# Performance work log

Measured on AMD Instinct MI355X. Metric: run time of the kernel, lower is better.

## Reference

```python
import jax, jax.numpy as jnp
import numpy as np

B, A, N = 8, 512, 64           # structures, atoms, neighbors
D, F, G = 128, 128, 25         # atom basis, filters, gaussians
L = 3                          # interaction blocks
GA = 512                       # angular feature dim = 2*n_zetas*2*n_angular*n_zetas
MAXZ = 100
CUTOFF, START = 5.0, 1.2
LN2 = 0.6931471805599453


def ssp(x):
    # shifted softplus: ln(1+exp(x)) - ln(2)
    return jax.nn.softplus(x) - LN2


def setup_inputs() -> dict:
    key = jax.random.key(0)
    ks = jax.random.split(key, 16)
    atomic_numbers = jax.random.randint(ks[0], (B, A), 0, MAXZ, dtype=jnp.int32)
    positions = jax.random.normal(ks[1], (B, A, 3), dtype=jnp.float32) * 3.0
    neighbors = jax.random.randint(ks[2], (B, A, N), 0, A, dtype=jnp.int32)
    neighbor_mask = jax.random.randint(ks[3], (B, A, N), 0, 2, dtype=jnp.int32)
    G_i = jax.random.normal(ks[4], (B, A, GA), dtype=jnp.float32)
    s = 0.05
    embedding = jax.random.normal(ks[5], (MAXZ, D), dtype=jnp.float32) * 0.1
    embedding = embedding.at[0].set(0.0)  # padding_idx=0
    inp = {
        'atomic_numbers': atomic_numbers,
        'positions': positions,
        'neighbors': neighbors,
        'neighbor_mask': neighbor_mask,
        'G_i': G_i,
        'embedding': embedding,
        'filt_w1': jax.random.normal(ks[6], (L, G, F), dtype=jnp.float32) * s,
        'filt_b1': jnp.zeros((L, F), jnp.float32),
        'filt_w2': jax.random.normal(ks[7], (L, F, F), dtype=jnp.float32) * s,
        'filt_b2': jnp.zeros((L, F), jnp.float32),
        'in2f_w': jax.random.normal(ks[8], (L, D, F), dtype=jnp.float32) * s,
        'f2out_w': jax.random.normal(ks[9], (L, F, D), dtype=jnp.float32) * s,
        'f2out_b': jnp.zeros((L, D), jnp.float32),
        'dense_w': jax.random.normal(ks[10], (L, D, D), dtype=jnp.float32) * s,
        'dense_b': jnp.zeros((L, D), jnp.float32),
        'ang_w': jax.random.normal(ks[11], (L, GA, D), dtype=jnp.float32) * s,
    }
    return inp


def reference(atomic_numbers, positions, neighbors, neighbor_mask, G_i,
              embedding, filt_w1, filt_b1, filt_w2, filt_b2,
              in2f_w, f2out_w, f2out_b, dense_w, dense_b, ang_w):
    gather = jax.vmap(lambda feat, idx: feat[idx])  # per-structure neighbor gather

    x = embedding[atomic_numbers]                    # [B,A,D]

    # AtomDistances: gather neighbor positions and take pairwise norms
    pos_j = gather(positions, neighbors)             # [B,A,N,3]
    dvec = pos_j - positions[:, :, None, :]
    r_ij = jnp.sqrt(jnp.sum(dvec * dvec, axis=-1) + 1e-12)  # [B,A,N]

    # GaussianSmearing(start, cutoff, n_gaussians)
    offsets = jnp.linspace(START, CUTOFF, G).astype(x.dtype)
    width = offsets[1] - offsets[0]
    f_ij = jnp.exp((-0.5 / (width * width)) * (r_ij[..., None] - offsets) ** 2)  # [B,A,N,G]

    C = (r_ij <= CUTOFF).astype(x.dtype)             # HardCutoff [B,A,N]
    mask = neighbor_mask.astype(x.dtype)             # [B,A,N]

    for l in range(in2f_w.shape[0]):
        # filter-generating network on expanded distances, modulated by cutoff
        W = ssp(f_ij @ filt_w1[l] + filt_b1[l]) @ filt_w2[l] + filt_b2[l]  # [B,A,N,F]
        W = W * C[..., None]
        # CFConv: project, gather neighbors, filter-weight, masked neighbor sum
        y = x @ in2f_w[l]                            # [B,A,F]
        y_j = gather(y, neighbors)                   # [B,A,N,F]
        agg = jnp.sum(y_j * W * mask[..., None], axis=2)  # [B,A,F]
        v_rad = agg @ f2out_w[l] + f2out_b[l]        # f2out (activation=None)
        v_rad = v_rad @ dense_w[l] + dense_b[l]      # self.dense
        v_ang = G_i @ ang_w[l]                       # dense_angular (no bias)
        x = x + ssp(v_rad + v_ang)                   # residual interaction update
    return x
```

## Files before the change

### kernel.cpp

```cpp
#include <hip/hip_runtime.h>
#include <math.h>

#define NB 8
#define NA 512
#define NN 64
#define ND 128
#define NF 128
#define NG 25
#define NGA 512
#define TABN 1024

typedef __attribute__((ext_vector_type(8))) short bf16x8;
typedef __attribute__((ext_vector_type(4))) float f32x4;

__device__ __forceinline__ float sspf(float v) {
  return fmaxf(v, 0.0f) + __logf(1.0f + __expf(-fabsf(v))) - 0.6931471805599453f;
}

__device__ __forceinline__ short f2bf(float x) {
  union { float f; unsigned u; } v; v.f = x;
  unsigned r = v.u + 0x7fffu + ((v.u >> 16) & 1u);
  return (short)(r >> 16);
}

#if defined(__has_builtin)
#if __has_builtin(__builtin_amdgcn_cvt_pk_bf16_f32)
#define HAS_PKBF 1
#endif
#endif

__device__ __forceinline__ unsigned pk2bf(float a, float b) {
#ifdef HAS_PKBF
  typedef __attribute__((ext_vector_type(2))) __bf16 v2bf;
  union { v2bf v; unsigned u; } c;
  c.v = __builtin_amdgcn_cvt_pk_bf16_f32(a, b);
  return c.u;
#else
  union { float f; unsigned u; } x, y; x.f = a; y.f = b;
  const unsigned ra = (x.u + 0x7fffu + ((x.u >> 16) & 1u)) >> 16;
  const unsigned rb = (y.u + 0x7fffu + ((y.u >> 16) & 1u)) & 0xffff0000u;
  return ra | rb;
#endif
}

__device__ __forceinline__ float bf2f(unsigned short us) {
  union { unsigned u; float f; } v; v.u = ((unsigned)us) << 16; return v.f;
}

__device__ __forceinline__ bf16x8 pack8(float4 a, float4 b) {
  bf16x8 r;
  unsigned* p = (unsigned*)&r;
  p[0] = pk2bf(a.x, a.y); p[1] = pk2bf(a.z, a.w);
  p[2] = pk2bf(b.x, b.y); p[3] = pk2bf(b.z, b.w);
  return r;
}

__device__ __forceinline__ bf16x8 fragT(const float* __restrict__ M, int ldn,
                                        int n, int k0q) {
  float e[8];
#pragma unroll
  for (int i = 0; i < 8; ++i) e[i] = M[(size_t)(k0q + i) * ldn + n];
  bf16x8 r; unsigned* p = (unsigned*)&r;
  p[0] = pk2bf(e[0], e[1]); p[1] = pk2bf(e[2], e[3]);
  p[2] = pk2bf(e[4], e[5]); p[3] = pk2bf(e[6], e[7]);
  return r;
}

__device__ __forceinline__ bf16x8 fragT25(const float* __restrict__ M,
                                          int n, int k0q) {
  float e[8];
#pragma unroll
  for (int i = 0; i < 8; ++i)
    e[i] = (k0q + i < NG) ? M[(size_t)(k0q + i) * NF + n] : 0.0f;
  bf16x8 r; unsigned* p = (unsigned*)&r;
  p[0] = pk2bf(e[0], e[1]); p[1] = pk2bf(e[2], e[3]);
  p[2] = pk2bf(e[4], e[5]); p[3] = pk2bf(e[6], e[7]);
  return r;
}

#define B_TT 48
#define B_AT (B_TT + 192)
#define B_PF (B_AT + 24)
#define B_TAB (B_PF + 192)
#define P1_TOT (B_TAB + 1024)

__global__ __launch_bounds__(256) void k_prep1(
    const float* __restrict__ fw1, const float* __restrict__ fb1,
    const float* __restrict__ fw2, const float* __restrict__ fb2,
    const float* __restrict__ in2f, const float* __restrict__ aw,
    const float* __restrict__ f2o, const float* __restrict__ f2ob,
    const float* __restrict__ dw, const float* __restrict__ db,
    const float* __restrict__ pos, const int* __restrict__ nbr,
    const int* __restrict__ nmask,
    short* __restrict__ in2fT, short* __restrict__ awT,
    short* __restrict__ W12T, float* __restrict__ b12,
    float* __restrict__ Ttab, int4* __restrict__ ent,
    int* __restrict__ nvArr) {
  __shared__ alignas(16) short sTile[32][33];
  __shared__ alignas(16) short sH[16 * 136];
  __shared__ alignas(16) int4 sCmp[4][NN];
  const int bx = blockIdx.x;
  const int t = threadIdx.x;
  const int lane = t & 63, wave = t >> 6;
  const int lanelo = lane & 15, quad = lane >> 4;
  const int wbase = wave << 5;

  if (bx < B_AT) {
    const float* src; short* dst; int tk0, tn0, stride;
    if (bx < B_TT) {
      const int l = bx >> 4, tile = bx & 15;
      src = in2f + (size_t)l * 16384;
      dst = in2fT + (size_t)l * 16384;
      tk0 = (tile >> 2) << 5; tn0 = (tile & 3) << 5; stride = 128;
    } else {
      const int ab = bx - B_TT;
      const int l = ab >> 6, tile = ab & 63;
      src = aw + (size_t)l * 65536;
      dst = awT + (size_t)l * 65536;
      tk0 = (tile >> 2) << 5; tn0 = (tile & 3) << 5; stride = 512;
    }
    const int tr = t >> 3, tc4 = (t & 7) << 2;
    const float4 v = *(const float4*)(src + (size_t)(tk0 + tr) * 128 + tn0 + tc4);
    sTile[tr][tc4] = f2bf(v.x); sTile[tr][tc4 + 1] = f2bf(v.y);
    sTile[tr][tc4 + 2] = f2bf(v.z); sTile[tr][tc4 + 3] = f2bf(v.w);
    __syncthreads();
    short o[4];
#pragma unroll
    for (int j = 0; j < 4; ++j) o[j] = sTile[tc4 + j][tr];
    uint2 pk;
    pk.x = ((unsigned)(unsigned short)o[0]) | (((unsigned)(unsigned short)o[1]) << 16);
    pk.y = ((unsigned)(unsigned short)o[2]) | (((unsigned)(unsigned short)o[3]) << 16);
    *(uint2*)(dst + (size_t)(tn0 + tr) * stride + tk0 + tc4) = pk;
    return;
  }
  if (bx < B_PF) {
    const int fb = bx - B_AT;
    const int l = fb >> 3, xi = fb & 7;
    const int i = (xi << 4) + lanelo;
    const float* f2o_l = f2o + (size_t)l * 16384;
    const float* dw_l = dw + (size_t)l * 16384;
    short* W12T_l = W12T + (size_t)l * 16384;
    f32x4 c[2] = {{0.f, 0.f, 0.f, 0.f}, {0.f, 0.f, 0.f, 0.f}};
#pragma unroll
    for (int kt = 0; kt < 4; ++kt) {
      const int k0 = kt * 32 + quad * 8;
      const bf16x8 b = pack8(*(const float4*)(f2o_l + (size_t)i * 128 + k0),
                             *(const float4*)(f2o_l + (size_t)i * 128 + k0 + 4));
#pragma unroll
      for (int ct = 0; ct < 2; ++ct) {
        const bf16x8 a = fragT(dw_l, 128, wbase + ct * 16 + lanelo, k0);
        c[ct] = __builtin_amdgcn_mfma_f32_16x16x32_bf16(a, b, c[ct], 0, 0, 0);
      }
    }
#pragma unroll
    for (int ct = 0; ct < 2; ++ct)
#pragma unroll
      for (int reg = 0; reg < 4; ++reg) {
        const int j = wbase + ct * 16 + quad * 4 + reg;
        W12T_l[(size_t)j * 128 + i] = f2bf(c[ct][reg]);
      }
    if (xi == 0 && t < 128) {
      float acc = db[(size_t)l * 128 + t];
      for (int k = 0; k < 128; ++k)
        acc += f2ob[(size_t)l * 128 + k] * dw_l[(size_t)k * 128 + t];
      b12[(size_t)l * 128 + t] = acc;
    }
    return;
  }
  if (bx < B_TAB) {
    const int tb = bx - B_PF;
    const int l = tb >> 6;
    const int chunk = tb & 63;
    const float* fw1_l = fw1 + (size_t)l * NG * NF;
    const float* fw2_l = fw2 + (size_t)l * 16384;
    const float* b1 = fb1 + (size_t)l * NF;
    const float* b2 = fb2 + (size_t)l * NF;

    float4 b1v[2];
    float b2r[2];
#pragma unroll
    for (int ct = 0; ct < 2; ++ct) {
      b1v[ct] = *(const float4*)(b1 + wbase + ct * 16 + quad * 4);
      b2r[ct] = b2[wbase + ct * 16 + lanelo];
    }

    const float stepg = 3.8f / 24.0f;
    const float coef = -0.5f / (stepg * stepg);
    const float rv = (float)(chunk * 16 + lanelo) * (5.0f / 1023.0f);
    bf16x8 gb;
    {
      float e[8];
#pragma unroll
      for (int i = 0; i < 8; ++i) {
        const int g = quad * 8 + i;
        const float d = rv - (1.2f + stepg * (float)g);
        e[i] = (g < NG) ? __expf(coef * d * d) : 0.0f;
      }
      unsigned* gp = (unsigned*)&gb;
      gp[0] = pk2bf(e[0], e[1]); gp[1] = pk2bf(e[2], e[3]);
      gp[2] = pk2bf(e[4], e[5]); gp[3] = pk2bf(e[6], e[7]);
    }
#pragma unroll
    for (int ct = 0; ct < 2; ++ct) {
      const bf16x8 a = fragT25(fw1_l, wbase + ct * 16 + lanelo, quad * 8);
      f32x4 c = {0.f, 0.f, 0.f, 0.f};
      c = __builtin_amdgcn_mfma_f32_16x16x32_bf16(a, gb, c, 0, 0, 0);
      const int f0 = wbase + ct * 16 + quad * 4;
      uint2 pk;
      pk.x = pk2bf(sspf(c[0] + b1v[ct].x), sspf(c[1] + b1v[ct].y));
      pk.y = pk2bf(sspf(c[2] + b1v[ct].z), sspf(c[3] + b1v[ct].w));
      *(uint2*)(sH + lanelo * 136 + f0) = pk;
    }
    __syncthreads();
    f32x4 acc[2];
    acc[0] = (f32x4){b2r[0], b2r[0], b2r[0], b2r[0]};
    acc[1] = (f32x4){b2r[1], b2r[1], b2r[1], b2r[1]};
#pragma unroll
    for (int kt = 0; kt < 4; ++kt) {
      const bf16x8 ah = *(const bf16x8*)(sH + lanelo * 136 + kt * 32 + quad * 8);
#pragma unroll
      for (int ct = 0; ct < 2; ++ct) {
        const bf16x8 a = fragT(fw2_l, 128, wbase + ct * 16 + lanelo, kt * 32 + quad * 8);
        acc[ct] = __builtin_amdgcn_mfma_f32_16x16x32_bf16(ah, a, acc[ct], 0, 0, 0);
      }
    }
#pragma unroll
    for (int ct = 0; ct < 2; ++ct)
#pragma unroll
      for (int reg = 0; reg < 4; ++reg) {
        const int rrow = chunk * 16 + quad * 4 + reg;
        const int f = wbase + ct * 16 + lanelo;
        Ttab[((size_t)l * TABN + rrow) * NF + f] = acc[ct][reg];
      }
    return;
  }
  {
    const int ga = (bx - B_TAB) * 4 + wave;
    const int b0 = ga & ~(NA - 1);
    const int nj = nbr[(size_t)ga * NN + lane];
    const int mk = nmask[(size_t)ga * NN + lane];
    const float px = pos[(size_t)ga * 3];
    const float py = pos[(size_t)ga * 3 + 1];
    const float pz = pos[(size_t)ga * 3 + 2];
    const float* pj = pos + (size_t)(b0 + nj) * 3;
    const float dx = pj[0] - px, dy = pj[1] - py, dz = pj[2] - pz;
    const float r = sqrtf(dx * dx + dy * dy + dz * dz + 1e-12f);
    const bool valid = (r <= 5.0f) && (mk != 0);
    const unsigned long long m = __ballot(valid);
    const int posc = __popcll(m & ((1ull << lane) - 1ull));
    const float tt = r * ((float)(TABN - 1) / 5.0f);
    int k0 = (int)tt; if (k0 > TABN - 2) k0 = TABN - 2;
    const float fr = tt - (float)k0;
    sCmp[wave][lane] = make_int4(0, b0 * NF, 0, 0);
    if (valid)
      sCmp[wave][posc] = make_int4(k0 * NF, (b0 + nj) * NF,
                                   __float_as_int(1.0f - fr), __float_as_int(fr));
    ent[(size_t)ga * NN + lane] = sCmp[wave][lane];
    if (lane == 0) nvArr[ga] = (int)__popcll(m);
  }
}

__global__ __launch_bounds__(256) void k_prep2(
    const float* __restrict__ emb, const int* __restrict__ zn,
    const short* __restrict__ in2fT,
    float* __restrict__ x, short* __restrict__ yB) {
  const int bx = blockIdx.x;
  const int t = threadIdx.x;
  const int lane = t & 63, wave = t >> 6;
  const int lanelo = lane & 15, quad = lane >> 4;
  const int wbase = wave << 5;

  const int row = (bx << 4) + lanelo;
  const float* erow = emb + (size_t)zn[row] * ND;
  f32x4 c[2] = {{0.f, 0.f, 0.f, 0.f}, {0.f, 0.f, 0.f, 0.f}};
#pragma unroll
  for (int kt = 0; kt < 4; ++kt) {
    const int k0 = kt * 32 + quad * 8;
    const float4 e0 = *(const float4*)(erow + k0);
    const float4 e1 = *(const float4*)(erow + k0 + 4);
    if (wave == 0) {
      *(float4*)(x + (size_t)row * ND + k0) = e0;
      *(float4*)(x + (size_t)row * ND + k0 + 4) = e1;
    }
    const bf16x8 b = pack8(e0, e1);
#pragma unroll
    for (int ct = 0; ct < 2; ++ct) {
      const bf16x8 a = *(const bf16x8*)(in2fT + (size_t)(wbase + ct * 16 + lanelo) * 128 + k0);
      c[ct] = __builtin_amdgcn_mfma_f32_16x16x32_bf16(a, b, c[ct], 0, 0, 0);
    }
  }
#pragma unroll
  for (int ct = 0; ct < 2; ++ct) {
    const int c0 = wbase + ct * 16 + quad * 4;
    uint2 pk; pk.x = pk2bf(c[ct][0], c[ct][1]); pk.y = pk2bf(c[ct][2], c[ct][3]);
    *(uint2*)(yB + (size_t)row * 128 + c0) = pk;
  }
}

__global__ __launch_bounds__(512, 4) void k_layer(
    const short* __restrict__ yIn, const float* __restrict__ Tt,
    const float* __restrict__ Gi, const short* __restrict__ awTl,
    float* __restrict__ x,
    const short* __restrict__ W12Tl, const float* __restrict__ b12l,
    const short* __restrict__ in2fTn, short* __restrict__ yOut,
    const int4* __restrict__ ent, const int* __restrict__ nvArr) {
  __shared__ alignas(16) int4 sEnt[8][NN];
  __shared__ alignas(16) float sAgg[16][136];
  __shared__ alignas(16) short sT[16 * 136];
  __shared__ alignas(16) short sGi[8][520];

  const int t = threadIdx.x;
  const int lane = t & 63;
  const int wave = t >> 6;
  const int lanelo = lane & 15;
  const int quad = lane >> 4;
  const int ga0 = blockIdx.x << 3;

  {
    const int r = t >> 6, cc = (t & 63) << 3;
    const float* g = Gi + (size_t)(ga0 + r) * NGA + cc;
    const bf16x8 v = pack8(*(const float4*)g, *(const float4*)(g + 4));
    *(bf16x8*)(&sGi[r][cc]) = v;
  }

  sEnt[wave][lane] = ent[(size_t)(ga0 + wave) * NN + lane];
  const int nv = nvArr[ga0 + wave];

  const unsigned short* yu = (const unsigned short*)yIn;
  float acc0 = 0.f, acc1 = 0.f;
  const int ntc = (nv + 3) & ~3;
  for (int c = 0; c < ntc; c += 4) {
#pragma unroll
    for (int u = 0; u < 4; ++u) {
      const int4 e = sEnt[wave][c + u];
      const float w0 = __int_as_float(e.z), w1 = __int_as_float(e.w);
      const float t0a = Tt[e.x + lane];
      const float t0b = Tt[e.x + lane + 64];
      const float t1a = Tt[e.x + NF + lane];
      const float t1b = Tt[e.x + NF + lane + 64];
      const float wva = fmaf(w0, t0a, w1 * t1a);
      const float wvb = fmaf(w0, t0b, w1 * t1b);
      acc0 = fmaf(wva, bf2f(yu[e.y + lane]), acc0);
      acc1 = fmaf(wvb, bf2f(yu[e.y + lane + 64]), acc1);
    }
  }
  sAgg[wave][lane] = acc0;
  sAgg[wave][lane + 64] = acc1;
  __syncthreads();

  f32x4 c2 = {0.f, 0.f, 0.f, 0.f};
#pragma unroll
  for (int kt = 0; kt < 4; ++kt) {
    const float* ar = &sAgg[lanelo][kt * 32 + quad * 8];
    const bf16x8 b = pack8(*(const float4*)ar, *(const float4*)(ar + 4));
    const bf16x8 a = *(const bf16x8*)(W12Tl + ((wave << 4) + lanelo) * 128 + kt * 32 + quad * 8);
    c2 = __builtin_amdgcn_mfma_f32_16x16x32_bf16(a, b, c2, 0, 0, 0);
  }
#pragma unroll 4
  for (int kt = 0; kt < 16; ++kt) {
    const int k0 = kt * 32 + quad * 8;
    const bf16x8 a = *(const bf16x8*)(awTl + (size_t)((wave << 4) + lanelo) * 512 + k0);
    const bf16x8 b = *(const bf16x8*)(&sGi[lanelo & 7][k0]);
    c2 = __builtin_amdgcn_mfma_f32_16x16x32_bf16(a, b, c2, 0, 0, 0);
  }

  const int c0 = (wave << 4) + quad * 4;
  const int row = ga0 + lanelo;
  if (lanelo < 8) {
    const float4 dv = *(const float4*)(b12l + c0);
    float* xp = x + (size_t)row * 128 + c0;
    const float4 xv = *(const float4*)xp;
    float4 xo;
    xo.x = xv.x + sspf(c2[0] + dv.x);
    xo.y = xv.y + sspf(c2[1] + dv.y);
    xo.z = xv.z + sspf(c2[2] + dv.z);
    xo.w = xv.w + sspf(c2[3] + dv.w);
    *(float4*)xp = xo;
    if (in2fTn != nullptr) {
      uint2 pk; pk.x = pk2bf(xo.x, xo.y); pk.y = pk2bf(xo.z, xo.w);
      *(uint2*)(sT + lanelo * 136 + c0) = pk;
    }
  }
  if (in2fTn == nullptr) return;
  __syncthreads();

  f32x4 c3 = {0.f, 0.f, 0.f, 0.f};
#pragma unroll
  for (int kt = 0; kt < 4; ++kt) {
    const bf16x8 b = *(const bf16x8*)(sT + lanelo * 136 + kt * 32 + quad * 8);
    const bf16x8 a = *(const bf16x8*)(in2fTn + ((wave << 4) + lanelo) * 128 + kt * 32 + quad * 8);
    c3 = __builtin_amdgcn_mfma_f32_16x16x32_bf16(a, b, c3, 0, 0, 0);
  }
  if (lanelo < 8) {
    uint2 pk; pk.x = pk2bf(c3[0], c3[1]); pk.y = pk2bf(c3[2], c3[3]);
    *(uint2*)(yOut + (size_t)row * 128 + c0) = pk;
  }
}

extern "C" void kernel_launch(void* const* d_in, const int* in_sizes, int n_in,
                              void* d_out, int out_size, void* d_ws, size_t ws_size,
                              hipStream_t stream) {
  (void)in_sizes; (void)n_in; (void)out_size; (void)ws_size;
  const int* zn = (const int*)d_in[0];
  const float* pos = (const float*)d_in[1];
  const int* nbr = (const int*)d_in[2];
  const int* nmask = (const int*)d_in[3];
  const float* Gi = (const float*)d_in[4];
  const float* emb = (const float*)d_in[5];
  const float* fw1 = (const float*)d_in[6];
  const float* fb1 = (const float*)d_in[7];
  const float* fw2 = (const float*)d_in[8];
  const float* fb2 = (const float*)d_in[9];
  const float* in2f = (const float*)d_in[10];
  const float* f2o = (const float*)d_in[11];
  const float* f2ob = (const float*)d_in[12];
  const float* dwp = (const float*)d_in[13];
  const float* dbp = (const float*)d_in[14];
  const float* awp = (const float*)d_in[15];

  float* x = (float*)d_out;
  float* b12 = (float*)d_ws;
  float* Ttab = b12 + 3 * 128;
  short* yA = (short*)(Ttab + (size_t)3 * TABN * NF);
  short* yBb = yA + (size_t)NB * NA * NF;
  short* in2fT = yBb + (size_t)NB * NA * NF;
  short* W12T = in2fT + (size_t)3 * 128 * 128;
  short* awT = W12T + (size_t)3 * 128 * 128;
  int4* ent = (int4*)(awT + (size_t)3 * 128 * 512);
  int* nvArr = (int*)(ent + (size_t)NB * NA * NN);

  k_prep1<<<P1_TOT, 256, 0, stream>>>(
      fw1, fb1, fw2, fb2, in2f, awp, f2o, f2ob, dwp, dbp,
      pos, nbr, nmask,
      in2fT, awT, W12T, b12, Ttab, ent, nvArr);
  k_prep2<<<NB * NA / 16, 256, 0, stream>>>(
      emb, zn, in2fT, x, yA);

  short* yin = yA;
  short* yout = yBb;
  for (int l = 0; l < 3; ++l) {
    k_layer<<<NB * NA / 8, 512, 0, stream>>>(yin,
        Ttab + (size_t)l * TABN * NF,
        Gi, awT + (size_t)l * 65536,
        x, W12T + (size_t)l * 16384, b12 + (size_t)l * 128,
        (l < 2) ? (in2fT + (size_t)(l + 1) * 16384) : nullptr, yout,
        ent, nvArr);
    short* tmp = yin; yin = yout; yout = tmp;
  }
}
```

Before: 151.7 us.

## Merge prep kernels into one launch and batch neighbor-entry work per wave

The two preprocessing kernels become a single launch. The initial y = emb·in2f[0] projection now reads in2f directly through strided fragT loads instead of waiting on a transposed bf16 copy, so only layers 1 and 2 still get transposed. Block order is rearranged so the heavy table-building blocks come first. The neighbor-entry blocks now handle four atoms per wave, cutting that block count by four. This removes one kernel launch and the dependency between the two prep stages, at the cost of uncoalesced weight reads in the y0 path.

Result: faster. 148.5 us (-2.1%).

```diff
diff --git a/kernel.cpp b/kernel.cpp
--- a/kernel.cpp
+++ b/kernel.cpp
@@ -78,13 +78,14 @@
   return r;
 }
 
-#define B_TT 48
-#define B_AT (B_TT + 192)
+#define B_TAB 192
+#define B_AT (B_TAB + 192)
 #define B_PF (B_AT + 24)
-#define B_TAB (B_PF + 192)
-#define P1_TOT (B_TAB + 1024)
-
-__global__ __launch_bounds__(256) void k_prep1(
+#define B_TT (B_PF + 32)
+#define B_Y0 (B_TT + 256)
+#define P_TOT (B_Y0 + 256)
+
+__global__ __launch_bounds__(256) void k_prep(
     const float* __restrict__ fw1, const float* __restrict__ fb1,
     const float* __restrict__ fw2, const float* __restrict__ fb2,
     const float* __restrict__ in2f, const float* __restrict__ aw,
@@ -92,10 +93,12 @@
     const float* __restrict__ dw, const float* __restrict__ db,
     const float* __restrict__ pos, const int* __restrict__ nbr,
     const int* __restrict__ nmask,
+    const float* __restrict__ emb, const int* __restrict__ zn,
     short* __restrict__ in2fT, short* __restrict__ awT,
     short* __restrict__ W12T, float* __restrict__ b12,
     float* __restrict__ Ttab, int4* __restrict__ ent,
-    int* __restrict__ nvArr) {
+    int* __restrict__ nvArr, float* __restrict__ x,
+    short* __restrict__ yB) {
   __shared__ alignas(16) short sTile[32][33];
   __shared__ alignas(16) short sH[16 * 136];
   __shared__ alignas(16) int4 sCmp[4][NN];
@@ -105,72 +108,9 @@
   const int lanelo = lane & 15, quad = lane >> 4;
   const int wbase = wave << 5;
 
-  if (bx < B_AT) {
-    const float* src; short* dst; int tk0, tn0, stride;
-    if (bx < B_TT) {
-      const int l = bx >> 4, tile = bx & 15;
-      src = in2f + (size_t)l * 16384;
-      dst = in2fT + (size_t)l * 16384;
-      tk0 = (tile >> 2) << 5; tn0 = (tile & 3) << 5; stride = 128;
-    } else {
-      const int ab = bx - B_TT;
-      const int l = ab >> 6, tile = ab & 63;
-      src = aw + (size_t)l * 65536;
-      dst = awT + (size_t)l * 65536;
-      tk0 = (tile >> 2) << 5; tn0 = (tile & 3) << 5; stride = 512;
-    }
-    const int tr = t >> 3, tc4 = (t & 7) << 2;
-    const float4 v = *(const float4*)(src + (size_t)(tk0 + tr) * 128 + tn0 + tc4);
-    sTile[tr][tc4] = f2bf(v.x); sTile[tr][tc4 + 1] = f2bf(v.y);
-    sTile[tr][tc4 + 2] = f2bf(v.z); sTile[tr][tc4 + 3] = f2bf(v.w);
-    __syncthreads();
-    short o[4];
-#pragma unroll
-    for (int j = 0; j < 4; ++j) o[j] = sTile[tc4 + j][tr];
-    uint2 pk;
-    pk.x = ((unsigned)(unsigned short)o[0]) | (((unsigned)(unsigned short)o[1]) << 16);
-    pk.y = ((unsigned)(unsigned short)o[2]) | (((unsigned)(unsigned short)o[3]) << 16);
-    *(uint2*)(dst + (size_t)(tn0 + tr) * stride + tk0 + tc4) = pk;
-    return;
-  }
-  if (bx < B_PF) {
-    const int fb = bx - B_AT;
-    const int l = fb >> 3, xi = fb & 7;
-    const int i = (xi << 4) + lanelo;
-    const float* f2o_l = f2o + (size_t)l * 16384;
-    const float* dw_l = dw + (size_t)l * 16384;
-    short* W12T_l = W12T + (size_t)l * 16384;
-    f32x4 c[2] = {{0.f, 0.f, 0.f, 0.f}, {0.f, 0.f, 0.f, 0.f}};
-#pragma unroll
-    for (int kt = 0; kt < 4; ++kt) {
-      const int k0 = kt * 32 + quad * 8;
-      const bf16x8 b = pack8(*(const float4*)(f2o_l + (size_t)i * 128 + k0),
-                             *(const float4*)(f2o_l + (size_t)i * 128 + k0 + 4));
-#pragma unroll
-      for (int ct = 0; ct < 2; ++ct) {
-        const bf16x8 a = fragT(dw_l, 128, wbase + ct * 16 + lanelo, k0);
-        c[ct] = __builtin_amdgcn_mfma_f32_16x16x32_bf16(a, b, c[ct], 0, 0, 0);
-      }
-    }
-#pragma unroll
-    for (int ct = 0; ct < 2; ++ct)
-#pragma unroll
-      for (int reg = 0; reg < 4; ++reg) {
-        const int j = wbase + ct * 16 + quad * 4 + reg;
-        W12T_l[(size_t)j * 128 + i] = f2bf(c[ct][reg]);
-      }
-    if (xi == 0 && t < 128) {
-      float acc = db[(size_t)l * 128 + t];
-      for (int k = 0; k < 128; ++k)
-        acc += f2ob[(size_t)l * 128 + k] * dw_l[(size_t)k * 128 + t];
-      b12[(size_t)l * 128 + t] = acc;
-    }
-    return;
-  }
   if (bx < B_TAB) {
-    const int tb = bx - B_PF;
-    const int l = tb >> 6;
-    const int chunk = tb & 63;
+    const int l = bx >> 6;
+    const int chunk = bx & 63;
     const float* fw1_l = fw1 + (size_t)l * NG * NF;
     const float* fw2_l = fw2 + (size_t)l * 16384;
     const float* b1 = fb1 + (size_t)l * NF;
@@ -234,66 +174,135 @@
       }
     return;
   }
+  if (bx < B_PF) {
+    if (bx < B_AT) {
+      const int ab = bx - B_TAB;
+      const int l = ab >> 6, tile = ab & 63;
+      const int tk0 = (tile >> 2) << 5, tn0 = (tile & 3) << 5;
+      const float* src = aw + (size_t)l * 65536;
+      short* dst = awT + (size_t)l * 65536;
+      const int tr = t >> 3, tc4 = (t & 7) << 2;
+      const float4 v = *(const float4*)(src + (size_t)(tk0 + tr) * 128 + tn0 + tc4);
+      sTile[tr][tc4] = f2bf(v.x); sTile[tr][tc4 + 1] = f2bf(v.y);
+      sTile[tr][tc4 + 2] = f2bf(v.z); sTile[tr][tc4 + 3] = f2bf(v.w);
+      __syncthreads();
+      short o[4];
+#pragma unroll
+      for (int j = 0; j < 4; ++j) o[j] = sTile[tc4 + j][tr];
+      uint2 pk;
+      pk.x = ((unsigned)(unsigned short)o[0]) | (((unsigned)(unsigned short)o[1]) << 16);
+      pk.y = ((unsigned)(unsigned short)o[2]) | (((unsigned)(unsigned short)o[3]) << 16);
+      *(uint2*)(dst + (size_t)(tn0 + tr) * 512 + tk0 + tc4) = pk;
+      return;
+    }
+    const int fb = bx - B_AT;
+    const int l = fb >> 3, xi = fb & 7;
+    const int i = (xi << 4) + lanelo;
+    const float* f2o_l = f2o + (size_t)l * 16384;
+    const float* dw_l = dw + (size_t)l * 16384;
+    short* W12T_l = W12T + (size_t)l * 16384;
+    f32x4 c[2] = {{0.f, 0.f, 0.f, 0.f}, {0.f, 0.f, 0.f, 0.f}};
+#pragma unroll
+    for (int kt = 0; kt < 4; ++kt) {
+      const int k0 = kt * 32 + quad * 8;
+      const bf16x8 b = pack8(*(const float4*)(f2o_l + (size_t)i * 128 + k0),
+                             *(const float4*)(f2o_l + (size_t)i * 128 + k0 + 4));
+#pragma unroll
+      for (int ct = 0; ct < 2; ++ct) {
+        const bf16x8 a = fragT(dw_l, 128, wbase + ct * 16 + lanelo, k0);
+        c[ct] = __builtin_amdgcn_mfma_f32_16x16x32_bf16(a, b, c[ct], 0, 0, 0);
+      }
+    }
+#pragma unroll
+    for (int ct = 0; ct < 2; ++ct)
+#pragma unroll
+      for (int reg = 0; reg < 4; ++reg) {
+        const int j = wbase + ct * 16 + quad * 4 + reg;
+        W12T_l[(size_t)j * 128 + i] = f2bf(c[ct][reg]);
+      }
+    if (xi == 0 && t < 128) {
+      float acc = db[(size_t)l * 128 + t];
+      for (int k = 0; k < 128; ++k)
+        acc += f2ob[(size_t)l * 128 + k] * dw_l[(size_t)k * 128 + t];
+      b12[(size_t)l * 128 + t] = acc;
+    }
+    return;
+  }
+  if (bx < B_TT) {
+    const int m = bx - B_PF;
+    const int l = 1 + (m >> 4), tile = m & 15;
+    const float* src = in2f + (size_t)l * 16384;
+    short* dst = in2fT + (size_t)l * 16384;
+    const int tk0 = (tile >> 2) << 5, tn0 = (tile & 3) << 5;
+    const int tr = t >> 3, tc4 = (t & 7) << 2;
+    const float4 v = *(const float4*)(src + (size_t)(tk0 + tr) * 128 + tn0 + tc4);
+    sTile[tr][tc4] = f2bf(v.x); sTile[tr][tc4 + 1] = f2bf(v.y);
+    sTile[tr][tc4 + 2] = f2bf(v.z); sTile[tr][tc4 + 3] = f2bf(v.w);
+    __syncthreads();
+    short o[4];
+#pragma unroll
+    for (int j = 0; j < 4; ++j) o[j] = sTile[tc4 + j][tr];
+    uint2 pk;
+    pk.x = ((unsigned)(unsigned short)o[0]) | (((unsigned)(unsigned short)o[1]) << 16);
+    pk.y = ((unsigned)(unsigned short)o[2]) | (((unsigned)(unsigned short)o[3]) << 16);
+    *(uint2*)(dst + (size_t)(tn0 + tr) * 128 + tk0 + tc4) = pk;
+    return;
+  }
+  if (bx < B_Y0) {
+    const int row = ((bx - B_TT) << 4) + lanelo;
+    const float* erow = emb + (size_t)zn[row] * ND;
+    f32x4 c[2] = {{0.f, 0.f, 0.f, 0.f}, {0.f, 0.f, 0.f, 0.f}};
+#pragma unroll
+    for (int kt = 0; kt < 4; ++kt) {
+      const int k0 = kt * 32 + quad * 8;
+      const float4 e0 = *(const float4*)(erow + k0);
+      const float4 e1 = *(const float4*)(erow + k0 + 4);
+      if (wave == 0) {
+        *(float4*)(x + (size_t)row * ND + k0) = e0;
+        *(float4*)(x + (size_t)row * ND + k0 + 4) = e1;
+      }
+      const bf16x8 b = pack8(e0, e1);
+#pragma unroll
+      for (int ct = 0; ct < 2; ++ct) {
+        const bf16x8 a = fragT(in2f, 128, wbase + ct * 16 + lanelo, k0);
+        c[ct] = __builtin_amdgcn_mfma_f32_16x16x32_bf16(a, b, c[ct], 0, 0, 0);
+      }
+    }
+#pragma unroll
+    for (int ct = 0; ct < 2; ++ct) {
+      const int c0 = wbase + ct * 16 + quad * 4;
+      uint2 pk; pk.x = pk2bf(c[ct][0], c[ct][1]); pk.y = pk2bf(c[ct][2], c[ct][3]);
+      *(uint2*)(yB + (size_t)row * 128 + c0) = pk;
+    }
+    return;
+  }
   {
-    const int ga = (bx - B_TAB) * 4 + wave;
-    const int b0 = ga & ~(NA - 1);
-    const int nj = nbr[(size_t)ga * NN + lane];
-    const int mk = nmask[(size_t)ga * NN + lane];
-    const float px = pos[(size_t)ga * 3];
-    const float py = pos[(size_t)ga * 3 + 1];
-    const float pz = pos[(size_t)ga * 3 + 2];
-    const float* pj = pos + (size_t)(b0 + nj) * 3;
-    const float dx = pj[0] - px, dy = pj[1] - py, dz = pj[2] - pz;
-    const float r = sqrtf(dx * dx + dy * dy + dz * dz + 1e-12f);
-    const bool valid = (r <= 5.0f) && (mk != 0);
-    const unsigned long long m = __ballot(valid);
-    const int posc = __popcll(m & ((1ull << lane) - 1ull));
-    const float tt = r * ((float)(TABN - 1) / 5.0f);
-    int k0 = (int)tt; if (k0 > TABN - 2) k0 = TABN - 2;
-    const float fr = tt - (float)k0;
-    sCmp[wave][lane] = make_int4(0, b0 * NF, 0, 0);
-    if (valid)
-      sCmp[wave][posc] = make_int4(k0 * NF, (b0 + nj) * NF,
-                                   __float_as_int(1.0f - fr), __float_as_int(fr));
-    ent[(size_t)ga * NN + lane] = sCmp[wave][lane];
-    if (lane == 0) nvArr[ga] = (int)__popcll(m);
-  }
-}
-
-__global__ __launch_bounds__(256) void k_prep2(
-    const float* __restrict__ emb, const int* __restrict__ zn,
-    const short* __restrict__ in2fT,
-    float* __restrict__ x, short* __restrict__ yB) {
-  const int bx = blockIdx.x;
-  const int t = threadIdx.x;
-  const int lane = t & 63, wave = t >> 6;
-  const int lanelo = lane & 15, quad = lane >> 4;
-  const int wbase = wave << 5;
-
-  const int row = (bx << 4) + lanelo;
-  const float* erow = emb + (size_t)zn[row] * ND;
-  f32x4 c[2] = {{0.f, 0.f, 0.f, 0.f}, {0.f, 0.f, 0.f, 0.f}};
-#pragma unroll
-  for (int kt = 0; kt < 4; ++kt) {
-    const int k0 = kt * 32 + quad * 8;
-    const float4 e0 = *(const float4*)(erow + k0);
-    const float4 e1 = *(const float4*)(erow + k0 + 4);
-    if (wave == 0) {
-      *(float4*)(x + (size_t)row * ND + k0) = e0;
-      *(float4*)(x + (size_t)row * ND + k0 + 4) = e1;
-    }
-    const bf16x8 b = pack8(e0, e1);
-#pragma unroll
-    for (int ct = 0; ct < 2; ++ct) {
-      const bf16x8 a = *(const bf16x8*)(in2fT + (size_t)(wbase + ct * 16 + lanelo) * 128 + k0);
-      c[ct] = __builtin_amdgcn_mfma_f32_16x16x32_bf16(a, b, c[ct], 0, 0, 0);
-    }
-  }
-#pragma unroll
-  for (int ct = 0; ct < 2; ++ct) {
-    const int c0 = wbase + ct * 16 + quad * 4;
-    uint2 pk; pk.x = pk2bf(c[ct][0], c[ct][1]); pk.y = pk2bf(c[ct][2], c[ct][3]);
-    *(uint2*)(yB + (size_t)row * 128 + c0) = pk;
+    const int gaB = (bx - B_Y0) * 16 + wave * 4;
+#pragma unroll
+    for (int aa = 0; aa < 4; ++aa) {
+      const int ga = gaB + aa;
+      const int b0 = ga & ~(NA - 1);
+      const int nj = nbr[(size_t)ga * NN + lane];
+      const int mk = nmask[(size_t)ga * NN + lane];
+      const float px = pos[(size_t)ga * 3];
+      const float py = pos[(size_t)ga * 3 + 1];
+      const float pz = pos[(size_t)ga * 3 + 2];
+      const float* pj = pos + (size_t)(b0 + nj) * 3;
+      const float dx = pj[0] - px, dy = pj[1] - py, dz = pj[2] - pz;
+      const float r = sqrtf(dx * dx + dy * dy + dz * dz + 1e-12f);
+      const bool valid = (r <= 5.0f) && (mk != 0);
+      const unsigned long long m = __ballot(valid);
+      const int posc = __popcll(m & ((1ull << lane) - 1ull));
+      const float tt = r * ((float)(TABN - 1) / 5.0f);
+      int k0 = (int)tt; if (k0 > TABN - 2) k0 = TABN - 2;
+      const float fr = tt - (float)k0;
+      sCmp[wave][lane] = make_int4(0, b0 * NF, 0, 0);
+      if (valid)
+        sCmp[wave][posc] = make_int4(k0 * NF, (b0 + nj) * NF,
+                                     __float_as_int(1.0f - fr), __float_as_int(fr));
+      ent[(size_t)ga * NN + lane] = sCmp[wave][lane];
+      if (lane == 0) nvArr[ga] = (int)__popcll(m);
+    }
   }
 }
 
@@ -429,12 +438,10 @@
   int4* ent = (int4*)(awT + (size_t)3 * 128 * 512);
   int* nvArr = (int*)(ent + (size_t)NB * NA * NN);
 
-  k_prep1<<<P1_TOT, 256, 0, stream>>>(
+  k_prep<<<P_TOT, 256, 0, stream>>>(
       fw1, fb1, fw2, fb2, in2f, awp, f2o, f2ob, dwp, dbp,
-      pos, nbr, nmask,
-      in2fT, awT, W12T, b12, Ttab, ent, nvArr);
-  k_prep2<<<NB * NA / 16, 256, 0, stream>>>(
-      emb, zn, in2fT, x, yA);
+      pos, nbr, nmask, emb, zn,
+      in2fT, awT, W12T, b12, Ttab, ent, nvArr, x, yA);
 
   short* yin = yA;
   short* yout = yBb;
```
